# Kernel tuning notes

Hardware: AMD Instinct MI355X
Metric: run time of the kernel (lower is better)

## Reference

```python
import jax, jax.numpy as jnp
import numpy as np

SUB = 5      # icosphere subdivisions -> V = 10*4^5 + 2 = 10242
B = 16       # batch size
ZD = 32      # z_dim
HID = 64     # hidden_dim


def _create_icosphere(sub):
    t = (1.0 + np.sqrt(5.0)) / 2.0
    v = np.array([[-1, t, 0], [1, t, 0], [-1, -t, 0], [1, -t, 0], [0, -1, t], [0, 1, t],
                  [0, -1, -t], [0, 1, -t], [t, 0, -1], [t, 0, 1], [-t, 0, -1], [-t, 0, 1]],
                 dtype=np.float32)
    v /= np.linalg.norm(v[0])
    f = np.array([[0, 11, 5], [0, 5, 1], [0, 1, 7], [0, 7, 10], [0, 10, 11], [1, 5, 9],
                  [5, 11, 4], [11, 10, 2], [10, 7, 6], [7, 1, 8], [3, 9, 4], [3, 4, 2],
                  [3, 2, 6], [3, 6, 8], [3, 8, 9], [4, 9, 5], [2, 4, 11], [6, 2, 10],
                  [8, 6, 7], [9, 8, 1]], dtype=np.int64)
    for _ in range(sub):
        mid = {}
        nv = list(v)
        nf = []
        def gm(i1, i2):
            k = (min(i1, i2), max(i1, i2))
            if k not in mid:
                m = (v[i1] + v[i2]) / 2.0
                m = m / np.linalg.norm(m)
                mid[k] = len(nv)
                nv.append(m)
            return mid[k]
        for v0, v1, v2 in f:
            a, b, c = gm(v0, v1), gm(v1, v2), gm(v2, v0)
            nf.extend([[v0, a, c], [v1, b, a], [v2, c, b], [a, b, c]])
        v = np.array(nv, dtype=np.float32)
        f = np.array(nf, dtype=np.int64)
    return v, f


def _adjacency(faces, nv):
    # symmetric edges + self loops, sym-normalized: 1/sqrt(deg[r]*deg[c])
    e = set()
    for a, b, c in faces:
        e.update([(int(a), int(b)), (int(b), int(a)), (int(b), int(c)),
                  (int(c), int(b)), (int(c), int(a)), (int(a), int(c))])
    for i in range(nv):
        e.add((i, i))
    e = np.array(sorted(e), dtype=np.int64)
    row, col = e[:, 0], e[:, 1]
    deg = np.bincount(row, minlength=nv).astype(np.float32)
    vals = (1.0 / np.sqrt(deg[row] * deg[col])).astype(np.float32)
    return row.astype(np.int32), col.astype(np.int32), vals


def _lin(key, din, dout):
    W = jax.random.normal(key, (dout, din), jnp.float32) / np.sqrt(din)
    b = jnp.zeros((dout,), jnp.float32)
    return W, b


def setup_inputs() -> dict:
    verts, faces = _create_icosphere(SUB)
    V = len(verts)
    row, col, vals = _adjacency(faces, V)
    template = jnp.asarray(verts)

    key = jax.random.key(0)
    ks = jax.random.split(key, 16)
    # input meshes = template + small deformation (realistic for this VAE)
    x = template[None] + 0.05 * jax.random.normal(ks[0], (B, V, 3), jnp.float32)
    eps = jax.random.normal(ks[1], (B, ZD), jnp.float32)

    W1, b1 = _lin(ks[2], 3, HID)
    W2, b2 = _lin(ks[3], HID, HID)
    W3, b3 = _lin(ks[4], HID, 2 * HID)
    Wfc, bfc = _lin(ks[5], 2 * HID, 4 * HID)
    Wmu, bmu = _lin(ks[6], 4 * HID, ZD)
    Wlv, blv = _lin(ks[7], 4 * HID, ZD)
    DH = 2 * HID  # decoder hidden_dim = 128
    Wd1, bd1 = _lin(ks[8], ZD + 3, DH)
    Wd2, bd2 = _lin(ks[9], DH, DH)
    Wd3, bd3 = _lin(ks[10], DH, DH // 2)
    Wd4, bd4 = _lin(ks[11], DH // 2, 3)

    return {"x": x, "eps": eps, "row": jnp.asarray(row), "col": jnp.asarray(col),
            "vals": jnp.asarray(vals), "template": template,
            "W1": W1, "b1": b1, "W2": W2, "b2": b2, "W3": W3, "b3": b3,
            "Wfc": Wfc, "bfc": bfc, "Wmu": Wmu, "bmu": bmu, "Wlv": Wlv, "blv": blv,
            "Wd1": Wd1, "bd1": bd1, "Wd2": Wd2, "bd2": bd2,
            "Wd3": Wd3, "bd3": bd3, "Wd4": Wd4, "bd4": bd4}


def _spmm(row, col, vals, h):
    # batched sparse (V,V) @ (B,V,C): out[b,r] = sum_e vals[e] * h[b, col[e]]
    msg = h[:, col, :] * vals[None, :, None]            # (B, E, C)
    return jnp.zeros(h.shape, h.dtype).at[:, row, :].add(msg)


def _linear(x, W, b):
    return x @ W.T + b


def reference(x, eps, row, col, vals, template,
              W1, b1, W2, b2, W3, b3, Wfc, bfc, Wmu, bmu, Wlv, blv,
              Wd1, bd1, Wd2, bd2, Wd3, bd3, Wd4, bd4):
    # --- encoder: 3 graph convs (linear -> spmm -> relu), mean pool, fc ---
    h = jax.nn.relu(_spmm(row, col, vals, _linear(x, W1, b1)))
    h = jax.nn.relu(_spmm(row, col, vals, _linear(h, W2, b2)))
    h = jax.nn.relu(_spmm(row, col, vals, _linear(h, W3, b3)))
    g = h.mean(axis=1)                                   # (B, 2*HID)
    feat = jax.nn.relu(_linear(g, Wfc, bfc))             # (B, 4*HID)
    mu = _linear(feat, Wmu, bmu)                         # (B, ZD)
    log_var = jnp.clip(_linear(feat, Wlv, blv), -20.0, 20.0)
    # --- reparameterize (eps supplied as input for determinism) ---
    z = mu + eps * jnp.exp(0.5 * log_var)
    # --- decoder MLP on [z, template] per vertex (dropout = eval mode) ---
    Bn, V = x.shape[0], template.shape[0]
    z_exp = jnp.broadcast_to(z[:, None, :], (Bn, V, z.shape[-1]))
    t_exp = jnp.broadcast_to(template[None], (Bn, V, 3))
    hd = jnp.concatenate([z_exp, t_exp], axis=-1)        # (B, V, ZD+3)
    hd = jax.nn.relu(_linear(hd, Wd1, bd1))
    hd = jax.nn.relu(_linear(hd, Wd2, bd2))
    hd = jax.nn.relu(_linear(hd, Wd3, bd3))
    offsets = _linear(hd, Wd4, bd4)                      # (B, V, 3)
    recon = template[None] + offsets
    return recon, mu, log_var
```

## Files before the change

### kernel.cpp

```cpp
#include <hip/hip_runtime.h>
#include <hip/hip_bf16.h>

typedef __attribute__((ext_vector_type(8))) unsigned short ushort8;
typedef __attribute__((ext_vector_type(4))) unsigned short ushort4v;
typedef __attribute__((ext_vector_type(8))) short short8v;
typedef __attribute__((ext_vector_type(4))) float f32x4;

__device__ __forceinline__ float bf2f(unsigned short u){
  union { unsigned int i; float f; } x; x.i = ((unsigned int)u) << 16; return x.f;
}
__device__ __forceinline__ unsigned short f2bf(float f){
  __hip_bfloat16 h = __float2bfloat16(f);
  return *reinterpret_cast<unsigned short*>(&h);
}

__global__ void prep_k(const int* __restrict__ row, const int* __restrict__ colx,
                       const float* __restrict__ vals, int nnz,
                       int* __restrict__ col7, float* __restrict__ val7,
                       float* __restrict__ dvec, float* __restrict__ g, int V, int GN){
  int v = blockIdx.x*256 + threadIdx.x;
  if (v < GN) g[v] = 0.f;
  if (v >= V) return;
  int lo = 0, hi = nnz;
  while (lo < hi){ int m = (lo+hi)>>1; if (row[m] < v) lo = m+1; else hi = m; }
  int e0 = lo;
  int lo2 = e0; hi = nnz;
  while (lo2 < hi){ int m = (lo2+hi)>>1; if (row[m] < v+1) lo2 = m+1; else hi = m; }
  int e1 = lo2;
  float s = 0.f;
  #pragma unroll
  for (int i=0;i<7;i++){
    int e = e0 + i;
    int c  = (e < e1) ? colx[e] : 0;
    float wv = (e < e1) ? vals[e] : 0.f;
    col7[v*7+i] = c; val7[v*7+i] = wv; s += wv;
  }
  dvec[v] = s;
}

__global__ void spmm_lin1_k(const float* __restrict__ x, const int* __restrict__ col7,
    const float* __restrict__ val7, const float* __restrict__ d,
    const float* __restrict__ W1, const float* __restrict__ b1,
    unsigned short* __restrict__ out, int V, int R){
  __shared__ float sW[192];
  __shared__ float sB[64];
  int tid = threadIdx.x;
  if (tid < 192) sW[tid] = W1[tid];
  if (tid < 64)  sB[tid] = b1[tid];
  __syncthreads();
  int r = blockIdx.x*256 + tid;
  if (r >= R) return;
  int b = r / V; int v = r - b*V;
  const float* xb = x + (size_t)b*V*3;
  int   cs[7]; float ws[7];
  #pragma unroll
  for (int i=0;i<7;i++){ cs[i] = col7[v*7+i]; ws[i] = val7[v*7+i]; }
  float s0=0.f, s1=0.f, s2=0.f;
  #pragma unroll
  for (int i=0;i<7;i++){
    const float* xr = xb + (size_t)cs[i]*3;
    s0 += ws[i]*xr[0]; s1 += ws[i]*xr[1]; s2 += ws[i]*xr[2];
  }
  float dv = d[v];
  unsigned short* orow = out + (size_t)r*64;
  #pragma unroll
  for (int cg=0; cg<8; ++cg){
    ushort8 o;
    #pragma unroll
    for (int k=0;k<8;k++){
      int c = cg*8 + k;
      float acc = dv*sB[c] + s0*sW[c*3] + s1*sW[c*3+1] + s2*sW[c*3+2];
      o[k] = f2bf(fmaxf(acc, 0.f));
    }
    *reinterpret_cast<ushort8*>(orow + cg*8) = o;
  }
}

__global__ __launch_bounds__(256) void spmm8s_k(const unsigned short* __restrict__ in,
    unsigned short* __restrict__ out, const int* __restrict__ col7,
    const float* __restrict__ val7, int V, int NBperB){
  int p = blockIdx.x;
  int xcd = p & 7, q = p >> 3;
  int half = (q >= NBperB) ? 1 : 0;
  int off  = q - half*NBperB;
  int b = xcd + (half<<3);
  int j = off*256 + (int)threadIdx.x;
  if (j >= V*8) return;
  int cg = j & 7; int v = j >> 3;
  const unsigned short* base = in + (size_t)b*V*64 + cg*8;
  int cols[7]; float vv[7];
  #pragma unroll
  for (int i=0;i<7;i++){ cols[i] = col7[v*7+i]; vv[i] = val7[v*7+i]; }
  ushort8 g[7];
  #pragma unroll
  for (int i=0;i<7;i++) g[i] = *reinterpret_cast<const ushort8*>(base + (size_t)cols[i]*64);
  float acc[8];
  #pragma unroll
  for (int k=0;k<8;k++) acc[k] = 0.f;
  #pragma unroll
  for (int i=0;i<7;i++){
    float s = vv[i];
    #pragma unroll
    for (int k=0;k<8;k++) acc[k] += s*bf2f(g[i][k]);
  }
  ushort8 o;
  #pragma unroll
  for (int k=0;k<8;k++) o[k] = f2bf(acc[k]);
  *reinterpret_cast<ushort8*>(out + ((size_t)b*V + v)*64 + cg*8) = o;
}

template<int K, int N, bool RELU, bool DBIAS>
__global__ __launch_bounds__(256) void lin_mfma_k(const unsigned short* __restrict__ in,
    const float* __restrict__ W, const float* __restrict__ bias,
    unsigned short* __restrict__ out, int R, const float* __restrict__ dvec, int V){
  constexpr int KP = K + 8;
  constexpr int NF = N / 16;
  constexpr int KS = K / 32;
  __shared__ unsigned short sW[N * KP];
  __shared__ float sB[N];
  int tid = threadIdx.x;
  for (int i = tid*4; i < N*K; i += 1024){
    const float4 wv = *reinterpret_cast<const float4*>(W + i);
    int n = i / K, k = i - n*K;
    unsigned short* dst = &sW[n*KP + k];
    dst[0] = f2bf(wv.x); dst[1] = f2bf(wv.y); dst[2] = f2bf(wv.z); dst[3] = f2bf(wv.w);
  }
  if (tid < N) sB[tid] = bias[tid];
  __syncthreads();

  const int wave = tid >> 6, lane = tid & 63;
  const int l15 = lane & 15, lg = lane >> 4;
  const int rbase = blockIdx.x*128 + wave*32;

  int r0c = min(rbase + l15,      R-1);
  int r1c = min(rbase + 16 + l15, R-1);
  const unsigned short* bp0 = in + (size_t)r0c*K + lg*8;
  const unsigned short* bp1 = in + (size_t)r1c*K + lg*8;
  const unsigned short* aBase = &sW[l15*KP + lg*8];

  f32x4 acc[NF][2];
  #pragma unroll
  for (int nf=0; nf<NF; ++nf){ acc[nf][0] = (f32x4)0.f; acc[nf][1] = (f32x4)0.f; }

  #pragma unroll
  for (int ks=0; ks<KS; ++ks){
    short8v b0 = *reinterpret_cast<const short8v*>(bp0 + ks*32);
    short8v b1 = *reinterpret_cast<const short8v*>(bp1 + ks*32);
    #pragma unroll
    for (int nf=0; nf<NF; ++nf){
      short8v a = *reinterpret_cast<const short8v*>(aBase + nf*16*KP + ks*32);
      acc[nf][0] = __builtin_amdgcn_mfma_f32_16x16x32_bf16(a, b0, acc[nf][0], 0,0,0);
      acc[nf][1] = __builtin_amdgcn_mfma_f32_16x16x32_bf16(a, b1, acc[nf][1], 0,0,0);
    }
  }

  #pragma unroll
  for (int rr=0; rr<2; ++rr){
    int r = rbase + rr*16 + l15;
    if (r >= R) continue;
    float bscale = 1.f;
    if (DBIAS){ int vv = r % V; bscale = dvec[vv]; }
    #pragma unroll
    for (int nf=0; nf<NF; ++nf){
      int nb = nf*16 + lg*4;
      ushort4v o;
      #pragma unroll
      for (int reg=0; reg<4; ++reg){
        float v = acc[nf][rr][reg] + bscale*sB[nb + reg];
        if (RELU) v = v > 0.f ? v : 0.f;
        o[reg] = f2bf(v);
      }
      *reinterpret_cast<ushort4v*>(out + (size_t)r*N + nb) = o;
    }
  }
}

__global__ __launch_bounds__(256) void lin3_mean_k(const unsigned short* __restrict__ in,
    const float* __restrict__ W, const float* __restrict__ bias,
    const float* __restrict__ dvec, float* __restrict__ g, int R, int V, int Bn){
  constexpr int K = 64, N = 128, KP = K + 8, NF = N/16, KS = K/32;
  __shared__ unsigned short sW[N * KP];
  __shared__ float sB[N];
  __shared__ float gPart[2][128];
  int tid = threadIdx.x;
  for (int i = tid*4; i < N*K; i += 1024){
    const float4 wv = *reinterpret_cast<const float4*>(W + i);
    int n = i / K, k = i - n*K;
    unsigned short* dst = &sW[n*KP + k];
    dst[0] = f2bf(wv.x); dst[1] = f2bf(wv.y); dst[2] = f2bf(wv.z); dst[3] = f2bf(wv.w);
  }
  if (tid < N) sB[tid] = bias[tid];
  if (tid < 128){ gPart[0][tid] = 0.f; gPart[1][tid] = 0.f; }
  __syncthreads();

  const int wave = tid >> 6, lane = tid & 63;
  const int l15 = lane & 15, lg = lane >> 4;
  const int rbase = blockIdx.x*128 + wave*32;

  int r0 = rbase + l15;
  int r1 = rbase + 16 + l15;
  int r0c = min(r0, R-1), r1c = min(r1, R-1);
  const unsigned short* bp0 = in + (size_t)r0c*K + lg*8;
  const unsigned short* bp1 = in + (size_t)r1c*K + lg*8;
  const unsigned short* aBase = &sW[l15*KP + lg*8];

  f32x4 acc[NF][2];
  #pragma unroll
  for (int nf=0; nf<NF; ++nf){ acc[nf][0] = (f32x4)0.f; acc[nf][1] = (f32x4)0.f; }

  #pragma unroll
  for (int ks=0; ks<KS; ++ks){
    short8v b0 = *reinterpret_cast<const short8v*>(bp0 + ks*32);
    short8v b1 = *reinterpret_cast<const short8v*>(bp1 + ks*32);
    #pragma unroll
    for (int nf=0; nf<NF; ++nf){
      short8v a = *reinterpret_cast<const short8v*>(aBase + nf*16*KP + ks*32);
      acc[nf][0] = __builtin_amdgcn_mfma_f32_16x16x32_bf16(a, b0, acc[nf][0], 0,0,0);
      acc[nf][1] = __builtin_amdgcn_mfma_f32_16x16x32_bf16(a, b1, acc[nf][1], 0,0,0);
    }
  }

  const int b0blk = (blockIdx.x*128) / V;
  bool ok0 = r0 < R, ok1 = r1 < R;
  int bb0 = r0c / V, bb1 = r1c / V;
  float d0 = dvec[r0c - bb0*V], d1 = dvec[r1c - bb1*V];
  bool in00 = ok0 && (bb0 == b0blk), in01 = ok0 && (bb0 == b0blk+1);
  bool in10 = ok1 && (bb1 == b0blk), in11 = ok1 && (bb1 == b0blk+1);

  #pragma unroll
  for (int nf=0; nf<NF; ++nf){
    #pragma unroll
    for (int reg=0; reg<4; ++reg){
      int c = nf*16 + lg*4 + reg;
      float v0 = fmaxf(acc[nf][0][reg] + d0*sB[c], 0.f);
      float v1 = fmaxf(acc[nf][1][reg] + d1*sB[c], 0.f);
      float sA = (in00 ? v0 : 0.f) + (in10 ? v1 : 0.f);
      float sBv= (in01 ? v0 : 0.f) + (in11 ? v1 : 0.f);
      #pragma unroll
      for (int m=1; m<16; m<<=1){
        sA  += __shfl_xor(sA,  m);
        sBv += __shfl_xor(sBv, m);
      }
      if (l15 == 0){
        atomicAdd(&gPart[0][c], sA);
        atomicAdd(&gPart[1][c], sBv);
      }
    }
  }
  __syncthreads();
  if (tid < 128){
    float a = gPart[0][tid];
    if (a != 0.f) atomicAdd(&g[b0blk*128 + tid], a);
    float b2 = gPart[1][tid];
    if (b2 != 0.f && b0blk+1 < Bn) atomicAdd(&g[(b0blk+1)*128 + tid], b2);
  }
}

__global__ __launch_bounds__(256) void head2_k(const float* __restrict__ g,
    const float* __restrict__ Wfc, const float* __restrict__ bfc,
    const float* __restrict__ Wmu, const float* __restrict__ bmu,
    const float* __restrict__ Wlv, const float* __restrict__ blv,
    const float* __restrict__ eps, const float* __restrict__ Wd1,
    const float* __restrict__ bd1, float* __restrict__ mu_out,
    float* __restrict__ lv_out, float* __restrict__ zp, float invV){
  int b = blockIdx.x;
  int tid = threadIdx.x;
  __shared__ float sG[128];
  __shared__ float sF[256];
  __shared__ float sMu[32];
  __shared__ float sLv[32];
  __shared__ float sZ[32];
  if (tid < 128) sG[tid] = g[b*128 + tid] * invV;
  __syncthreads();
  {
    const float4* wr = reinterpret_cast<const float4*>(Wfc + tid*128);
    float acc = bfc[tid];
    #pragma unroll 8
    for (int k4=0;k4<32;k4++){
      float4 wv = wr[k4];
      acc += sG[k4*4]*wv.x + sG[k4*4+1]*wv.y + sG[k4*4+2]*wv.z + sG[k4*4+3]*wv.w;
    }
    sF[tid] = fmaxf(acc, 0.f);
  }
  __syncthreads();
  if (tid < 64){
    int c = tid & 31;
    bool isMu = tid < 32;
    const float4* wr = reinterpret_cast<const float4*>((isMu ? Wmu : Wlv) + c*256);
    float acc = isMu ? bmu[c] : blv[c];
    #pragma unroll 8
    for (int k4=0;k4<64;k4++){
      float4 wv = wr[k4];
      acc += sF[k4*4]*wv.x + sF[k4*4+1]*wv.y + sF[k4*4+2]*wv.z + sF[k4*4+3]*wv.w;
    }
    if (isMu){ sMu[c] = acc; mu_out[b*32+c] = acc; }
    else {
      acc = fminf(20.f, fmaxf(-20.f, acc));
      sLv[c] = acc; lv_out[b*32+c] = acc;
    }
  }
  __syncthreads();
  if (tid < 32) sZ[tid] = sMu[tid] + eps[b*32+tid]*expf(0.5f*sLv[tid]);
  __syncthreads();
  if (tid < 128){
    const float* wr = Wd1 + tid*35;
    float acc = bd1[tid];
    #pragma unroll
    for (int k=0;k<32;k++) acc += sZ[k]*wr[k];
    zp[b*128 + tid] = acc;
  }
}

__global__ __launch_bounds__(256) void dec_k(const float* __restrict__ zp,
    const float* __restrict__ tmpl, const float* __restrict__ Wd1,
    const float* __restrict__ Wd2, const float* __restrict__ bd2,
    const float* __restrict__ Wd3, const float* __restrict__ bd3,
    const float* __restrict__ Wd4, const float* __restrict__ bd4,
    float* __restrict__ out, int R, int V){
  constexpr int KP = 152;
  __shared__ unsigned short sW[64*KP];
  __shared__ unsigned short sH[128*KP];
  __shared__ float sB2[128];
  __shared__ float sB3[64];
  __shared__ float sW4[192];
  __shared__ float sB4[3];
  __shared__ float sZP[16*128];
  __shared__ float sWT[128*3];
  int tid = threadIdx.x;

  if (tid < 128) sB2[tid] = bd2[tid];
  if (tid < 64)  sB3[tid] = bd3[tid];
  if (tid < 192) sW4[tid] = Wd4[tid];
  if (tid < 3)   sB4[tid] = bd4[tid];
  for (int i = tid; i < 16*128; i += 256) sZP[i] = zp[i];
  if (tid < 128){
    sWT[tid*3+0] = Wd1[tid*35+32];
    sWT[tid*3+1] = Wd1[tid*35+33];
    sWT[tid*3+2] = Wd1[tid*35+34];
  }
  auto stageW = [&](const float* Wsrc){
    for (int i = tid*4; i < 64*128; i += 1024){
      float4 wv = *reinterpret_cast<const float4*>(Wsrc + i);
      int n = i >> 7, k = i & 127;
      unsigned short* dst = &sW[n*KP + k];
      dst[0]=f2bf(wv.x); dst[1]=f2bf(wv.y); dst[2]=f2bf(wv.z); dst[3]=f2bf(wv.w);
    }
  };
  stageW(Wd2);
  __syncthreads();

  const int wave = tid >> 6, lane = tid & 63;
  const int l15 = lane & 15, lg = lane >> 4;
  const int rbase = blockIdx.x*128 + wave*32;
  const int lrow = wave*32;

  int r0c = min(rbase + l15,      R-1);
  int r1c = min(rbase + 16 + l15, R-1);
  int b0 = r0c / V, v0 = r0c - b0*V;
  int b1 = r1c / V, v1 = r1c - b1*V;
  float t0x=tmpl[v0*3], t0y=tmpl[v0*3+1], t0z=tmpl[v0*3+2];
  float t1x=tmpl[v1*3], t1y=tmpl[v1*3+1], t1z=tmpl[v1*3+2];

  short8v bf0[4], bf1[4];
  #pragma unroll
  for (int ks=0; ks<4; ++ks){
    #pragma unroll
    for (int k=0;k<8;k++){
      int c = lg*8 + ks*32 + k;
      const float* wt = &sWT[c*3];
      float h0 = sZP[b0*128+c] + t0x*wt[0]+t0y*wt[1]+t0z*wt[2];
      float h1 = sZP[b1*128+c] + t1x*wt[0]+t1y*wt[1]+t1z*wt[2];
      bf0[ks][k] = (short)f2bf(fmaxf(h0,0.f));
      bf1[ks][k] = (short)f2bf(fmaxf(h1,0.f));
    }
  }

  const unsigned short* aBase = &sW[l15*KP + lg*8];

  #pragma unroll
  for (int half=0; half<2; ++half){
    if (half==1){
      __syncthreads();
      stageW(Wd2 + 64*128);
      __syncthreads();
    }
    f32x4 acc[4][2];
    #pragma unroll
    for (int nf=0; nf<4; ++nf){ acc[nf][0]=(f32x4)0.f; acc[nf][1]=(f32x4)0.f; }
    #pragma unroll
    for (int ks=0; ks<4; ++ks){
      #pragma unroll
      for (int nf=0; nf<4; ++nf){
        short8v a = *reinterpret_cast<const short8v*>(aBase + nf*16*KP + ks*32);
        acc[nf][0] = __builtin_amdgcn_mfma_f32_16x16x32_bf16(a, bf0[ks], acc[nf][0], 0,0,0);
        acc[nf][1] = __builtin_amdgcn_mfma_f32_16x16x32_bf16(a, bf1[ks], acc[nf][1], 0,0,0);
      }
    }
    #pragma unroll
    for (int rr=0; rr<2; ++rr){
      #pragma unroll
      for (int nf=0; nf<4; ++nf){
        int c = half*64 + nf*16 + lg*4;
        ushort4v o;
        #pragma unroll
        for (int reg=0; reg<4; ++reg)
          o[reg] = f2bf(fmaxf(acc[nf][rr][reg] + sB2[c+reg], 0.f));
        *reinterpret_cast<ushort4v*>(&sH[(lrow + rr*16 + l15)*KP + c]) = o;
      }
    }
  }
  __syncthreads();
  stageW(Wd3);
  __syncthreads();

  f32x4 acc3[4][2];
  #pragma unroll
  for (int nf=0; nf<4; ++nf){ acc3[nf][0]=(f32x4)0.f; acc3[nf][1]=(f32x4)0.f; }
  #pragma unroll
  for (int ks=0; ks<4; ++ks){
    short8v h0 = *reinterpret_cast<const short8v*>(&sH[(lrow + l15)*KP + ks*32 + lg*8]);
    short8v h1 = *reinterpret_cast<const short8v*>(&sH[(lrow + 16 + l15)*KP + ks*32 + lg*8]);
    #pragma unroll
    for (int nf=0; nf<4; ++nf){
      short8v a = *reinterpret_cast<const short8v*>(aBase + nf*16*KP + ks*32);
      acc3[nf][0] = __builtin_amdgcn_mfma_f32_16x16x32_bf16(a, h0, acc3[nf][0], 0,0,0);
      acc3[nf][1] = __builtin_amdgcn_mfma_f32_16x16x32_bf16(a, h1, acc3[nf][1], 0,0,0);
    }
  }

  #pragma unroll
  for (int rr=0; rr<2; ++rr){
    int r = rbase + rr*16 + l15;
    float p0 = 0.f, p1 = 0.f, p2 = 0.f;
    #pragma unroll
    for (int nf=0; nf<4; ++nf){
      #pragma unroll
      for (int reg=0; reg<4; ++reg){
        int c = nf*16 + lg*4 + reg;
        float h = fmaxf(acc3[nf][rr][reg] + sB3[c], 0.f);
        p0 += h*sW4[c]; p1 += h*sW4[64+c]; p2 += h*sW4[128+c];
      }
    }
    p0 += __shfl_xor(p0,16); p0 += __shfl_xor(p0,32);
    p1 += __shfl_xor(p1,16); p1 += __shfl_xor(p1,32);
    p2 += __shfl_xor(p2,16); p2 += __shfl_xor(p2,32);
    if (lg == 0 && r < R){
      int v = rr ? v1 : v0;
      out[(size_t)r*3+0] = tmpl[v*3+0] + p0 + sB4[0];
      out[(size_t)r*3+1] = tmpl[v*3+1] + p1 + sB4[1];
      out[(size_t)r*3+2] = tmpl[v*3+2] + p2 + sB4[2];
    }
  }
}

extern "C" void kernel_launch(void* const* d_in, const int* in_sizes, int n_in,
                              void* d_out, int out_size, void* d_ws, size_t ws_size,
                              hipStream_t stream){
  const float* x    = (const float*)d_in[0];
  const float* eps  = (const float*)d_in[1];
  const int*   row  = (const int*)d_in[2];
  const int*   colx = (const int*)d_in[3];
  const float* vals = (const float*)d_in[4];
  const float* tmpl = (const float*)d_in[5];
  const float* W1 = (const float*)d_in[6];  const float* b1 = (const float*)d_in[7];
  const float* W2 = (const float*)d_in[8];  const float* b2 = (const float*)d_in[9];
  const float* W3 = (const float*)d_in[10]; const float* b3 = (const float*)d_in[11];
  const float* Wfc= (const float*)d_in[12]; const float* bfc= (const float*)d_in[13];
  const float* Wmu= (const float*)d_in[14]; const float* bmu= (const float*)d_in[15];
  const float* Wlv= (const float*)d_in[16]; const float* blv= (const float*)d_in[17];
  const float* Wd1= (const float*)d_in[18]; const float* bd1= (const float*)d_in[19];
  const float* Wd2= (const float*)d_in[20]; const float* bd2= (const float*)d_in[21];
  const float* Wd3= (const float*)d_in[22]; const float* bd3= (const float*)d_in[23];
  const float* Wd4= (const float*)d_in[24]; const float* bd4= (const float*)d_in[25];

  int V   = in_sizes[5] / 3;
  int Bn  = in_sizes[1] / 32;
  int nnz = in_sizes[2];
  int R   = Bn * V;

  char* w = (char*)d_ws;
  size_t off = 0;
  auto alloc = [&](size_t bytes)->char*{
    char* p = w + off; off = (off + bytes + 255) & ~(size_t)255; return p;
  };
  unsigned short* bufA = (unsigned short*)alloc((size_t)R * 64 * 2);
  unsigned short* bufB = (unsigned short*)alloc((size_t)R * 64 * 2);
  int*   col7 = (int*)alloc((size_t)V*7*4);
  float* val7 = (float*)alloc((size_t)V*7*4);
  float* dvec = (float*)alloc((size_t)V*4);
  float* g    = (float*)alloc((size_t)Bn*128*4);
  float* zpb  = (float*)alloc((size_t)Bn*128*4);

  float* recon  = (float*)d_out;
  float* mu_out = recon + (size_t)R*3;
  float* lv_out = mu_out + (size_t)Bn*32;

  int mfmaGrid = (R + 127) / 128;
  int NBperB = (V*8 + 255) / 256;

  prep_k<<<(V+255)/256, 256, 0, stream>>>(row, colx, vals, nnz, col7, val7, dvec, g, V, Bn*128);

  spmm_lin1_k<<<(R+255)/256, 256, 0, stream>>>(x, col7, val7, dvec, W1, b1, bufA, V, R);
  spmm8s_k<<<16*NBperB, 256, 0, stream>>>(bufA, bufB, col7, val7, V, NBperB);
  lin_mfma_k<64,64,true,true><<<mfmaGrid, 256, 0, stream>>>(bufB, W2, b2, bufA, R, dvec, V);
  spmm8s_k<<<16*NBperB, 256, 0, stream>>>(bufA, bufB, col7, val7, V, NBperB);
  lin3_mean_k<<<mfmaGrid, 256, 0, stream>>>(bufB, W3, b3, dvec, g, R, V, Bn);

  head2_k<<<Bn, 256, 0, stream>>>(g, Wfc, bfc, Wmu, bmu, Wlv, blv, eps, Wd1, bd1,
                                  mu_out, lv_out, zpb, 1.0f/(float)V);

  dec_k<<<mfmaGrid, 256, 0, stream>>>(zpb, tmpl, Wd1, Wd2, bd2, Wd3, bd3, Wd4, bd4,
                                      recon, R, V);
}
```

Baseline: 145.0 us.

## Apply XCD-aware batch-to-block swizzle to all per-vertex kernels

Every per-vertex kernel now decodes its block index into a (batch, vertex-tile) pair with the same XCD-interleaved mapping the SpMM kernel already used. All blocks of one batch then land on the same XCD, so each batch's activations stay in that XCD's L2 from one stage to the next. Because a tile never straddles two batches, the mean-pool kernel needs only one partial accumulator and the decoder loads one batch's latent projection instead of all sixteen. The cost is some padded tail blocks per batch (V is not a multiple of 128), and the mapping hard-codes 8 XCDs and B=16.

```diff
diff --git a/kernel.cpp b/kernel.cpp
--- a/kernel.cpp
+++ b/kernel.cpp
@@ -12,6 +12,13 @@
 __device__ __forceinline__ unsigned short f2bf(float f){
   __hip_bfloat16 h = __float2bfloat16(f);
   return *reinterpret_cast<unsigned short*>(&h);
+}
+
+__device__ __forceinline__ void sw_decode(int p, int NB, int& b, int& off){
+  int xcd = p & 7, q = p >> 3;
+  int hi = (q >= NB) ? 1 : 0;
+  b = xcd + (hi << 3);
+  off = q - (hi ? NB : 0);
 }
 
 __global__ void prep_k(const int* __restrict__ row, const int* __restrict__ colx,
@@ -41,16 +48,16 @@
 __global__ void spmm_lin1_k(const float* __restrict__ x, const int* __restrict__ col7,
     const float* __restrict__ val7, const float* __restrict__ d,
     const float* __restrict__ W1, const float* __restrict__ b1,
-    unsigned short* __restrict__ out, int V, int R){
+    unsigned short* __restrict__ out, int V, int NB){
   __shared__ float sW[192];
   __shared__ float sB[64];
   int tid = threadIdx.x;
   if (tid < 192) sW[tid] = W1[tid];
   if (tid < 64)  sB[tid] = b1[tid];
   __syncthreads();
-  int r = blockIdx.x*256 + tid;
-  if (r >= R) return;
-  int b = r / V; int v = r - b*V;
+  int b, off; sw_decode(blockIdx.x, NB, b, off);
+  int v = off*256 + tid;
+  if (v >= V) return;
   const float* xb = x + (size_t)b*V*3;
   int   cs[7]; float ws[7];
   #pragma unroll
@@ -62,7 +69,7 @@
     s0 += ws[i]*xr[0]; s1 += ws[i]*xr[1]; s2 += ws[i]*xr[2];
   }
   float dv = d[v];
-  unsigned short* orow = out + (size_t)r*64;
+  unsigned short* orow = out + ((size_t)b*V + v)*64;
   #pragma unroll
   for (int cg=0; cg<8; ++cg){
     ushort8 o;
@@ -78,12 +85,8 @@
 
 __global__ __launch_bounds__(256) void spmm8s_k(const unsigned short* __restrict__ in,
     unsigned short* __restrict__ out, const int* __restrict__ col7,
-    const float* __restrict__ val7, int V, int NBperB){
-  int p = blockIdx.x;
-  int xcd = p & 7, q = p >> 3;
-  int half = (q >= NBperB) ? 1 : 0;
-  int off  = q - half*NBperB;
-  int b = xcd + (half<<3);
+    const float* __restrict__ val7, int V, int NB){
+  int b, off; sw_decode(blockIdx.x, NB, b, off);
   int j = off*256 + (int)threadIdx.x;
   if (j >= V*8) return;
   int cg = j & 7; int v = j >> 3;
@@ -109,10 +112,10 @@
   *reinterpret_cast<ushort8*>(out + ((size_t)b*V + v)*64 + cg*8) = o;
 }
 
-template<int K, int N, bool RELU, bool DBIAS>
+template<int K, int N, bool RELU>
 __global__ __launch_bounds__(256) void lin_mfma_k(const unsigned short* __restrict__ in,
     const float* __restrict__ W, const float* __restrict__ bias,
-    unsigned short* __restrict__ out, int R, const float* __restrict__ dvec, int V){
+    unsigned short* __restrict__ out, const float* __restrict__ dvec, int V, int NB){
   constexpr int KP = K + 8;
   constexpr int NF = N / 16;
   constexpr int KS = K / 32;
@@ -128,14 +131,16 @@
   if (tid < N) sB[tid] = bias[tid];
   __syncthreads();
 
+  int b, off; sw_decode(blockIdx.x, NB, b, off);
   const int wave = tid >> 6, lane = tid & 63;
   const int l15 = lane & 15, lg = lane >> 4;
-  const int rbase = blockIdx.x*128 + wave*32;
-
-  int r0c = min(rbase + l15,      R-1);
-  int r1c = min(rbase + 16 + l15, R-1);
-  const unsigned short* bp0 = in + (size_t)r0c*K + lg*8;
-  const unsigned short* bp1 = in + (size_t)r1c*K + lg*8;
+  const int vbase = off*128 + wave*32;
+
+  int v0r = vbase + l15, v1r = vbase + 16 + l15;
+  int v0c = min(v0r, V-1), v1c = min(v1r, V-1);
+  const size_t bb = (size_t)b*V;
+  const unsigned short* bp0 = in + (bb + v0c)*K + lg*8;
+  const unsigned short* bp1 = in + (bb + v1c)*K + lg*8;
   const unsigned short* aBase = &sW[l15*KP + lg*8];
 
   f32x4 acc[NF][2];
@@ -154,34 +159,34 @@
     }
   }
 
+  float d0 = dvec[v0c], d1 = dvec[v1c];
   #pragma unroll
   for (int rr=0; rr<2; ++rr){
-    int r = rbase + rr*16 + l15;
-    if (r >= R) continue;
-    float bscale = 1.f;
-    if (DBIAS){ int vv = r % V; bscale = dvec[vv]; }
+    int v = rr ? v1r : v0r;
+    if (v >= V) continue;
+    float ds = rr ? d1 : d0;
     #pragma unroll
     for (int nf=0; nf<NF; ++nf){
       int nb = nf*16 + lg*4;
       ushort4v o;
       #pragma unroll
       for (int reg=0; reg<4; ++reg){
-        float v = acc[nf][rr][reg] + bscale*sB[nb + reg];
-        if (RELU) v = v > 0.f ? v : 0.f;
-        o[reg] = f2bf(v);
+        float val = acc[nf][rr][reg] + ds*sB[nb + reg];
+        if (RELU) val = val > 0.f ? val : 0.f;
+        o[reg] = f2bf(val);
       }
-      *reinterpret_cast<ushort4v*>(out + (size_t)r*N + nb) = o;
+      *reinterpret_cast<ushort4v*>(out + (bb + v)*N + nb) = o;
     }
   }
 }
 
 __global__ __launch_bounds__(256) void lin3_mean_k(const unsigned short* __restrict__ in,
     const float* __restrict__ W, const float* __restrict__ bias,
-    const float* __restrict__ dvec, float* __restrict__ g, int R, int V, int Bn){
+    const float* __restrict__ dvec, float* __restrict__ g, int V, int NB){
   constexpr int K = 64, N = 128, KP = K + 8, NF = N/16, KS = K/32;
   __shared__ unsigned short sW[N * KP];
   __shared__ float sB[N];
-  __shared__ float gPart[2][128];
+  __shared__ float gPart[128];
   int tid = threadIdx.x;
   for (int i = tid*4; i < N*K; i += 1024){
     const float4 wv = *reinterpret_cast<const float4*>(W + i);
@@ -190,18 +195,19 @@
     dst[0] = f2bf(wv.x); dst[1] = f2bf(wv.y); dst[2] = f2bf(wv.z); dst[3] = f2bf(wv.w);
   }
   if (tid < N) sB[tid] = bias[tid];
-  if (tid < 128){ gPart[0][tid] = 0.f; gPart[1][tid] = 0.f; }
-  __syncthreads();
-
+  if (tid < 128) gPart[tid] = 0.f;
+  __syncthreads();
+
+  int b, off; sw_decode(blockIdx.x, NB, b, off);
   const int wave = tid >> 6, lane = tid & 63;
   const int l15 = lane & 15, lg = lane >> 4;
-  const int rbase = blockIdx.x*128 + wave*32;
-
-  int r0 = rbase + l15;
-  int r1 = rbase + 16 + l15;
-  int r0c = min(r0, R-1), r1c = min(r1, R-1);
-  const unsigned short* bp0 = in + (size_t)r0c*K + lg*8;
-  const unsigned short* bp1 = in + (size_t)r1c*K + lg*8;
+  const int vbase = off*128 + wave*32;
+
+  int v0r = vbase + l15, v1r = vbase + 16 + l15;
+  int v0c = min(v0r, V-1), v1c = min(v1r, V-1);
+  const size_t bb = (size_t)b*V;
+  const unsigned short* bp0 = in + (bb + v0c)*K + lg*8;
+  const unsigned short* bp1 = in + (bb + v1c)*K + lg*8;
   const unsigned short* aBase = &sW[l15*KP + lg*8];
 
   f32x4 acc[NF][2];
@@ -220,39 +226,25 @@
     }
   }
 
-  const int b0blk = (blockIdx.x*128) / V;
-  bool ok0 = r0 < R, ok1 = r1 < R;
-  int bb0 = r0c / V, bb1 = r1c / V;
-  float d0 = dvec[r0c - bb0*V], d1 = dvec[r1c - bb1*V];
-  bool in00 = ok0 && (bb0 == b0blk), in01 = ok0 && (bb0 == b0blk+1);
-  bool in10 = ok1 && (bb1 == b0blk), in11 = ok1 && (bb1 == b0blk+1);
-
+  bool ok0 = v0r < V, ok1 = v1r < V;
+  float d0 = dvec[v0c], d1 = dvec[v1c];
   #pragma unroll
   for (int nf=0; nf<NF; ++nf){
     #pragma unroll
     for (int reg=0; reg<4; ++reg){
       int c = nf*16 + lg*4 + reg;
-      float v0 = fmaxf(acc[nf][0][reg] + d0*sB[c], 0.f);
-      float v1 = fmaxf(acc[nf][1][reg] + d1*sB[c], 0.f);
-      float sA = (in00 ? v0 : 0.f) + (in10 ? v1 : 0.f);
-      float sBv= (in01 ? v0 : 0.f) + (in11 ? v1 : 0.f);
+      float v0f = fmaxf(acc[nf][0][reg] + d0*sB[c], 0.f);
+      float v1f = fmaxf(acc[nf][1][reg] + d1*sB[c], 0.f);
+      float sA = (ok0 ? v0f : 0.f) + (ok1 ? v1f : 0.f);
       #pragma unroll
-      for (int m=1; m<16; m<<=1){
-        sA  += __shfl_xor(sA,  m);
-        sBv += __shfl_xor(sBv, m);
-      }
-      if (l15 == 0){
-        atomicAdd(&gPart[0][c], sA);
-        atomicAdd(&gPart[1][c], sBv);
-      }
+      for (int m=1; m<16; m<<=1) sA += __shfl_xor(sA, m);
+      if (l15 == 0) atomicAdd(&gPart[c], sA);
     }
   }
   __syncthreads();
   if (tid < 128){
-    float a = gPart[0][tid];
-    if (a != 0.f) atomicAdd(&g[b0blk*128 + tid], a);
-    float b2 = gPart[1][tid];
-    if (b2 != 0.f && b0blk+1 < Bn) atomicAdd(&g[(b0blk+1)*128 + tid], b2);
+    float a = gPart[tid];
+    if (a != 0.f) atomicAdd(&g[b*128 + tid], a);
   }
 }
 
@@ -316,7 +308,7 @@
     const float* __restrict__ Wd2, const float* __restrict__ bd2,
     const float* __restrict__ Wd3, const float* __restrict__ bd3,
     const float* __restrict__ Wd4, const float* __restrict__ bd4,
-    float* __restrict__ out, int R, int V){
+    float* __restrict__ out, int V, int NB){
   constexpr int KP = 152;
   __shared__ unsigned short sW[64*KP];
   __shared__ unsigned short sH[128*KP];
@@ -324,15 +316,16 @@
   __shared__ float sB3[64];
   __shared__ float sW4[192];
   __shared__ float sB4[3];
-  __shared__ float sZP[16*128];
+  __shared__ float sZPb[128];
   __shared__ float sWT[128*3];
   int tid = threadIdx.x;
+  int b, off; sw_decode(blockIdx.x, NB, b, off);
 
   if (tid < 128) sB2[tid] = bd2[tid];
   if (tid < 64)  sB3[tid] = bd3[tid];
   if (tid < 192) sW4[tid] = Wd4[tid];
   if (tid < 3)   sB4[tid] = bd4[tid];
-  for (int i = tid; i < 16*128; i += 256) sZP[i] = zp[i];
+  if (tid < 128) sZPb[tid] = zp[b*128 + tid];
   if (tid < 128){
     sWT[tid*3+0] = Wd1[tid*35+32];
     sWT[tid*3+1] = Wd1[tid*35+33];
@@ -351,13 +344,11 @@
 
   const int wave = tid >> 6, lane = tid & 63;
   const int l15 = lane & 15, lg = lane >> 4;
-  const int rbase = blockIdx.x*128 + wave*32;
+  const int vbase = off*128 + wave*32;
   const int lrow = wave*32;
 
-  int r0c = min(rbase + l15,      R-1);
-  int r1c = min(rbase + 16 + l15, R-1);
-  int b0 = r0c / V, v0 = r0c - b0*V;
-  int b1 = r1c / V, v1 = r1c - b1*V;
+  int v0r = vbase + l15, v1r = vbase + 16 + l15;
+  int v0 = min(v0r, V-1), v1 = min(v1r, V-1);
   float t0x=tmpl[v0*3], t0y=tmpl[v0*3+1], t0z=tmpl[v0*3+2];
   float t1x=tmpl[v1*3], t1y=tmpl[v1*3+1], t1z=tmpl[v1*3+2];
 
@@ -368,10 +359,9 @@
     for (int k=0;k<8;k++){
       int c = lg*8 + ks*32 + k;
       const float* wt = &sWT[c*3];
-      float h0 = sZP[b0*128+c] + t0x*wt[0]+t0y*wt[1]+t0z*wt[2];
-      float h1 = sZP[b1*128+c] + t1x*wt[0]+t1y*wt[1]+t1z*wt[2];
-      bf0[ks][k] = (short)f2bf(fmaxf(h0,0.f));
-      bf1[ks][k] = (short)f2bf(fmaxf(h1,0.f));
+      float zc = sZPb[c];
+      bf0[ks][k] = (short)f2bf(fmaxf(zc + t0x*wt[0]+t0y*wt[1]+t0z*wt[2], 0.f));
+      bf1[ks][k] = (short)f2bf(fmaxf(zc + t1x*wt[0]+t1y*wt[1]+t1z*wt[2], 0.f));
     }
   }
 
@@ -430,7 +420,7 @@
 
   #pragma unroll
   for (int rr=0; rr<2; ++rr){
-    int r = rbase + rr*16 + l15;
+    int vr = rr ? v1r : v0r;
     float p0 = 0.f, p1 = 0.f, p2 = 0.f;
     #pragma unroll
     for (int nf=0; nf<4; ++nf){
@@ -444,11 +434,11 @@
     p0 += __shfl_xor(p0,16); p0 += __shfl_xor(p0,32);
     p1 += __shfl_xor(p1,16); p1 += __shfl_xor(p1,32);
     p2 += __shfl_xor(p2,16); p2 += __shfl_xor(p2,32);
-    if (lg == 0 && r < R){
-      int v = rr ? v1 : v0;
-      out[(size_t)r*3+0] = tmpl[v*3+0] + p0 + sB4[0];
-      out[(size_t)r*3+1] = tmpl[v*3+1] + p1 + sB4[1];
-      out[(size_t)r*3+2] = tmpl[v*3+2] + p2 + sB4[2];
+    if (lg == 0 && vr < V){
+      size_t o = ((size_t)b*V + vr)*3;
+      out[o+0] = tmpl[vr*3+0] + p0 + sB4[0];
+      out[o+1] = tmpl[vr*3+1] + p1 + sB4[1];
+      out[o+2] = tmpl[vr*3+2] + p2 + sB4[2];
     }
   }
 }
@@ -495,20 +485,21 @@
   float* mu_out = recon + (size_t)R*3;
   float* lv_out = mu_out + (size_t)Bn*32;
 
-  int mfmaGrid = (R + 127) / 128;
-  int NBperB = (V*8 + 255) / 256;
+  int NB1 = (V + 255) / 256;
+  int NB8 = (V*8 + 255) / 256;
+  int NBm = (V + 127) / 128;
 
   prep_k<<<(V+255)/256, 256, 0, stream>>>(row, colx, vals, nnz, col7, val7, dvec, g, V, Bn*128);
 
-  spmm_lin1_k<<<(R+255)/256, 256, 0, stream>>>(x, col7, val7, dvec, W1, b1, bufA, V, R);
-  spmm8s_k<<<16*NBperB, 256, 0, stream>>>(bufA, bufB, col7, val7, V, NBperB);
-  lin_mfma_k<64,64,true,true><<<mfmaGrid, 256, 0, stream>>>(bufB, W2, b2, bufA, R, dvec, V);
-  spmm8s_k<<<16*NBperB, 256, 0, stream>>>(bufA, bufB, col7, val7, V, NBperB);
-  lin3_mean_k<<<mfmaGrid, 256, 0, stream>>>(bufB, W3, b3, dvec, g, R, V, Bn);
+  spmm_lin1_k<<<16*NB1, 256, 0, stream>>>(x, col7, val7, dvec, W1, b1, bufA, V, NB1);
+  spmm8s_k<<<16*NB8, 256, 0, stream>>>(bufA, bufB, col7, val7, V, NB8);
+  lin_mfma_k<64,64,true><<<16*NBm, 256, 0, stream>>>(bufB, W2, b2, bufA, dvec, V, NBm);
+  spmm8s_k<<<16*NB8, 256, 0, stream>>>(bufA, bufB, col7, val7, V, NB8);
+  lin3_mean_k<<<16*NBm, 256, 0, stream>>>(bufB, W3, b3, dvec, g, V, NBm);
 
   head2_k<<<Bn, 256, 0, stream>>>(g, Wfc, bfc, Wmu, bmu, Wlv, blv, eps, Wd1, bd1,
                                   mu_out, lv_out, zpb, 1.0f/(float)V);
 
-  dec_k<<<mfmaGrid, 256, 0, stream>>>(zpb, tmpl, Wd1, Wd2, bd2, Wd3, bd3, Wd4, bd4,
-                                      recon, R, V);
-}
+  dec_k<<<16*NBm, 256, 0, stream>>>(zpb, tmpl, Wd1, Wd2, bd2, Wd3, bd3, Wd4, bd4,
+                                    recon, V, NBm);
+}
```

Result: faster. 131.9 us (-9.1%).
